# Kernel optimization log

Hardware: AMD Instinct MI355X
Metric: run time of the kernel (lower is better)

## Reference

```python
import jax, jax.numpy as jnp
import numpy as np

N = 4_194_304  # number of Gaussian samples (rays * samples_per_ray)


def setup_inputs() -> dict:
    key = jax.random.key(0)
    k1, k2 = jax.random.split(key)
    # means spread around the unit sphere so mask (||x||>=1) is mixed
    mean = jax.random.normal(k1, (N, 3), dtype=jnp.float32)
    cov = jax.random.normal(k2, (N, 3, 3), dtype=jnp.float32)
    return {"mean": mean, "cov": cov}


def _contract(x):
    # f(x) = x if ||x||<=1 else (2 - 1/||x||) * x/||x||  (Frobenius norm, order=None)
    mag = jnp.linalg.norm(x, axis=-1, keepdims=True)
    return jnp.where(mag < 1, x, (2.0 - 1.0 / mag) * (x / mag))


def _contract_gauss(x):
    # branch-free contraction used for the Jacobian (matches torch contract_gauss)
    mag = jnp.linalg.norm(x, axis=-1, keepdims=True)
    return (2.0 - 1.0 / mag) * (x / mag)


def reference(mean, cov):
    means = _contract(mean)  # [N, 3]
    # per-sample 3x3 Jacobian of contract_gauss, mirroring torch.func.vmap(jacrev(...))
    jc = jax.vmap(jax.jacrev(_contract_gauss))(mean)  # [N, 3, 3]
    mag = jnp.linalg.norm(mean, axis=-1)  # [N]
    mask = mag >= 1.0
    # J @ cov @ J^T for masked samples; computed densely then selected (same math)
    new_cov = jnp.einsum("nij,njk,nlk->nil", jc, cov, jc)
    cov_out = jnp.where(mask[:, None, None], new_cov, cov)
    return means, cov_out
```

## Files before the change

kernel.cpp:

```cpp
#include <hip/hip_runtime.h>


#define BLOCK 256

__global__ __launch_bounds__(BLOCK) void scene_contraction_kernel(
    const float* __restrict__ mean,
    const float* __restrict__ cov,
    float* __restrict__ out_mean,
    float* __restrict__ out_cov,
    int N)
{
    __shared__ float sm[BLOCK * 3];
    __shared__ float sc[BLOCK * 9];

    const int tid = threadIdx.x;
    const long long bs = (long long)blockIdx.x * BLOCK;
    const bool full = (bs + BLOCK <= (long long)N);

    if (full) {
        const float4* gm4 = (const float4*)(mean + bs * 3);
        float4* sm4 = (float4*)sm;
        if (tid < 192) sm4[tid] = gm4[tid];

        const float4* gc4 = (const float4*)(cov + bs * 9);
        float4* sc4 = (float4*)sc;
        sc4[tid]        = gc4[tid];
        sc4[tid + 256]  = gc4[tid + 256];
        if (tid < 64) sc4[tid + 512] = gc4[tid + 512];
    } else {
        const long long m_end = (long long)N * 3 - bs * 3;
        for (int i = tid; i < BLOCK * 3; i += BLOCK)
            if (i < m_end) sm[i] = mean[bs * 3 + i];
        const long long c_end = (long long)N * 9 - bs * 9;
        for (int i = tid; i < BLOCK * 9; i += BLOCK)
            if (i < c_end) sc[i] = cov[bs * 9 + i];
    }
    __syncthreads();

    if (bs + tid < (long long)N) {
        const float x = sm[tid * 3 + 0];
        const float y = sm[tid * 3 + 1];
        const float z = sm[tid * 3 + 2];
        const float r2 = x * x + y * y + z * z;
        const float r = sqrtf(r2);

        if (r >= 1.0f) {
            const float inv  = 1.0f / r;
            const float s    = (2.0f - inv) * inv;
            const float inv2 = inv * inv;
            const float cc   = 2.0f * (1.0f - r) * (inv2 * inv2);

            const float j00 = fmaf(cc * x, x, s);
            const float j01 = cc * x * y;
            const float j02 = cc * x * z;
            const float j11 = fmaf(cc * y, y, s);
            const float j12 = cc * y * z;
            const float j22 = fmaf(cc * z, z, s);

            const float e0 = sc[tid * 9 + 0], e1 = sc[tid * 9 + 1], e2 = sc[tid * 9 + 2];
            const float e3 = sc[tid * 9 + 3], e4 = sc[tid * 9 + 4], e5 = sc[tid * 9 + 5];
            const float e6 = sc[tid * 9 + 6], e7 = sc[tid * 9 + 7], e8 = sc[tid * 9 + 8];

            const float t00 = j00 * e0 + j01 * e3 + j02 * e6;
            const float t01 = j00 * e1 + j01 * e4 + j02 * e7;
            const float t02 = j00 * e2 + j01 * e5 + j02 * e8;
            const float t10 = j01 * e0 + j11 * e3 + j12 * e6;
            const float t11 = j01 * e1 + j11 * e4 + j12 * e7;
            const float t12 = j01 * e2 + j11 * e5 + j12 * e8;
            const float t20 = j02 * e0 + j12 * e3 + j22 * e6;
            const float t21 = j02 * e1 + j12 * e4 + j22 * e7;
            const float t22 = j02 * e2 + j12 * e5 + j22 * e8;

            sc[tid * 9 + 0] = t00 * j00 + t01 * j01 + t02 * j02;
            sc[tid * 9 + 1] = t00 * j01 + t01 * j11 + t02 * j12;
            sc[tid * 9 + 2] = t00 * j02 + t01 * j12 + t02 * j22;
            sc[tid * 9 + 3] = t10 * j00 + t11 * j01 + t12 * j02;
            sc[tid * 9 + 4] = t10 * j01 + t11 * j11 + t12 * j12;
            sc[tid * 9 + 5] = t10 * j02 + t11 * j12 + t12 * j22;
            sc[tid * 9 + 6] = t20 * j00 + t21 * j01 + t22 * j02;
            sc[tid * 9 + 7] = t20 * j01 + t21 * j11 + t22 * j12;
            sc[tid * 9 + 8] = t20 * j02 + t21 * j12 + t22 * j22;

            sm[tid * 3 + 0] = s * x;
            sm[tid * 3 + 1] = s * y;
            sm[tid * 3 + 2] = s * z;
        }
    }
    __syncthreads();

    if (full) {
        float4* om4 = (float4*)(out_mean + bs * 3);
        const float4* sm4 = (const float4*)sm;
        if (tid < 192) om4[tid] = sm4[tid];

        float4* oc4 = (float4*)(out_cov + bs * 9);
        const float4* sc4 = (const float4*)sc;
        oc4[tid]        = sc4[tid];
        oc4[tid + 256]  = sc4[tid + 256];
        if (tid < 64) oc4[tid + 512] = sc4[tid + 512];
    } else {
        const long long m_end = (long long)N * 3 - bs * 3;
        for (int i = tid; i < BLOCK * 3; i += BLOCK)
            if (i < m_end) out_mean[bs * 3 + i] = sm[i];
        const long long c_end = (long long)N * 9 - bs * 9;
        for (int i = tid; i < BLOCK * 9; i += BLOCK)
            if (i < c_end) out_cov[bs * 9 + i] = sc[i];
    }
}

extern "C" void kernel_launch(void* const* d_in, const int* in_sizes, int n_in,
                              void* d_out, int out_size, void* d_ws, size_t ws_size,
                              hipStream_t stream) {
    const float* mean = (const float*)d_in[0];
    const float* cov  = (const float*)d_in[1];
    float* out        = (float*)d_out;

    const int N = in_sizes[0] / 3;
    float* out_mean = out;
    float* out_cov  = out + (size_t)N * 3;

    const int blocks = (N + BLOCK - 1) / BLOCK;
    hipLaunchKernelGGL(scene_contraction_kernel, dim3(blocks), dim3(BLOCK), 0, stream,
                       mean, cov, out_mean, out_cov, N);
}
```

Baseline: 331.8 us.

## Process four samples per thread with direct float4 loads, drop LDS staging

Replaces the shared-memory staging with per-thread register processing of four consecutive samples. Each thread loads 3 float4 of means and 9 float4 of covariance directly, and the contraction becomes branch-free via select. This removes the LDS round trip and barriers and increases loads in flight per thread. The cost is strided per-lane access within a wavefront, which may hurt coalescing, and higher register use.

```diff
diff --git a/kernel.cpp b/kernel.cpp
--- a/kernel.cpp
+++ b/kernel.cpp
@@ -2,6 +2,58 @@
 
 
 #define BLOCK 256
+
+union F12 { float4 v[3]; float f[12]; };
+union F36 { float4 v[9]; float f[36]; };
+
+__device__ __forceinline__ void contract_one(
+    float x, float y, float z,
+    const float* __restrict__ e,
+    float* __restrict__ om,
+    float* __restrict__ oc)
+{
+    const float r2 = fmaf(x, x, fmaf(y, y, z * z));
+    const float r  = sqrtf(r2);
+    const float inv = 1.0f / r;
+    float s  = (2.0f - inv) * inv;
+    const float inv2 = inv * inv;
+    float cc = 2.0f * (1.0f - r) * (inv2 * inv2);
+
+    const bool inside = r < 1.0f;
+    s  = inside ? 1.0f : s;
+    cc = inside ? 0.0f : cc;
+
+    const float j00 = fmaf(cc * x, x, s);
+    const float j01 = cc * x * y;
+    const float j02 = cc * x * z;
+    const float j11 = fmaf(cc * y, y, s);
+    const float j12 = cc * y * z;
+    const float j22 = fmaf(cc * z, z, s);
+
+    om[0] = s * x;
+    om[1] = s * y;
+    om[2] = s * z;
+
+    const float t00 = j00 * e[0] + j01 * e[3] + j02 * e[6];
+    const float t01 = j00 * e[1] + j01 * e[4] + j02 * e[7];
+    const float t02 = j00 * e[2] + j01 * e[5] + j02 * e[8];
+    const float t10 = j01 * e[0] + j11 * e[3] + j12 * e[6];
+    const float t11 = j01 * e[1] + j11 * e[4] + j12 * e[7];
+    const float t12 = j01 * e[2] + j11 * e[5] + j12 * e[8];
+    const float t20 = j02 * e[0] + j12 * e[3] + j22 * e[6];
+    const float t21 = j02 * e[1] + j12 * e[4] + j22 * e[7];
+    const float t22 = j02 * e[2] + j12 * e[5] + j22 * e[8];
+
+    oc[0] = t00 * j00 + t01 * j01 + t02 * j02;
+    oc[1] = t00 * j01 + t01 * j11 + t02 * j12;
+    oc[2] = t00 * j02 + t01 * j12 + t02 * j22;
+    oc[3] = t10 * j00 + t11 * j01 + t12 * j02;
+    oc[4] = t10 * j01 + t11 * j11 + t12 * j12;
+    oc[5] = t10 * j02 + t11 * j12 + t12 * j22;
+    oc[6] = t20 * j00 + t21 * j01 + t22 * j02;
+    oc[7] = t20 * j01 + t21 * j11 + t22 * j12;
+    oc[8] = t20 * j02 + t21 * j12 + t22 * j22;
+}
 
 __global__ __launch_bounds__(BLOCK) void scene_contraction_kernel(
     const float* __restrict__ mean,
@@ -10,101 +62,43 @@
     float* __restrict__ out_cov,
     int N)
 {
-    __shared__ float sm[BLOCK * 3];
-    __shared__ float sc[BLOCK * 9];
+    const long long t  = (long long)blockIdx.x * BLOCK + threadIdx.x;
+    const long long s0 = t * 4;
+    if (s0 >= N) return;
 
-    const int tid = threadIdx.x;
-    const long long bs = (long long)blockIdx.x * BLOCK;
-    const bool full = (bs + BLOCK <= (long long)N);
+    if (s0 + 4 <= N) {
+        F12 m;  F36 c;
+        const float4* mg = (const float4*)mean + t * 3;
+        const float4* cg = (const float4*)cov  + t * 9;
+        #pragma unroll
+        for (int i = 0; i < 3; ++i) m.v[i] = mg[i];
+        #pragma unroll
+        for (int i = 0; i < 9; ++i) c.v[i] = cg[i];
 
-    if (full) {
-        const float4* gm4 = (const float4*)(mean + bs * 3);
-        float4* sm4 = (float4*)sm;
-        if (tid < 192) sm4[tid] = gm4[tid];
+        F12 om; F36 oc;
+        #pragma unroll
+        for (int k = 0; k < 4; ++k)
+            contract_one(m.f[3*k], m.f[3*k+1], m.f[3*k+2],
+                         &c.f[9*k], &om.f[3*k], &oc.f[9*k]);
 
-        const float4* gc4 = (const float4*)(cov + bs * 9);
-        float4* sc4 = (float4*)sc;
-        sc4[tid]        = gc4[tid];
-        sc4[tid + 256]  = gc4[tid + 256];
-        if (tid < 64) sc4[tid + 512] = gc4[tid + 512];
+        float4* omg = (float4*)out_mean + t * 3;
+        float4* ocg = (float4*)out_cov  + t * 9;
+        #pragma unroll
+        for (int i = 0; i < 3; ++i) omg[i] = om.v[i];
+        #pragma unroll
+        for (int i = 0; i < 9; ++i) ocg[i] = oc.v[i];
     } else {
-        const long long m_end = (long long)N * 3 - bs * 3;
-        for (int i = tid; i < BLOCK * 3; i += BLOCK)
-            if (i < m_end) sm[i] = mean[bs * 3 + i];
-        const long long c_end = (long long)N * 9 - bs * 9;
-        for (int i = tid; i < BLOCK * 9; i += BLOCK)
-            if (i < c_end) sc[i] = cov[bs * 9 + i];
-    }
-    __syncthreads();
-
-    if (bs + tid < (long long)N) {
-        const float x = sm[tid * 3 + 0];
-        const float y = sm[tid * 3 + 1];
-        const float z = sm[tid * 3 + 2];
-        const float r2 = x * x + y * y + z * z;
-        const float r = sqrtf(r2);
-
-        if (r >= 1.0f) {
-            const float inv  = 1.0f / r;
-            const float s    = (2.0f - inv) * inv;
-            const float inv2 = inv * inv;
-            const float cc   = 2.0f * (1.0f - r) * (inv2 * inv2);
-
-            const float j00 = fmaf(cc * x, x, s);
-            const float j01 = cc * x * y;
-            const float j02 = cc * x * z;
-            const float j11 = fmaf(cc * y, y, s);
-            const float j12 = cc * y * z;
-            const float j22 = fmaf(cc * z, z, s);
-
-            const float e0 = sc[tid * 9 + 0], e1 = sc[tid * 9 + 1], e2 = sc[tid * 9 + 2];
-            const float e3 = sc[tid * 9 + 3], e4 = sc[tid * 9 + 4], e5 = sc[tid * 9 + 5];
-            const float e6 = sc[tid * 9 + 6], e7 = sc[tid * 9 + 7], e8 = sc[tid * 9 + 8];
-
-            const float t00 = j00 * e0 + j01 * e3 + j02 * e6;
-            const float t01 = j00 * e1 + j01 * e4 + j02 * e7;
-            const float t02 = j00 * e2 + j01 * e5 + j02 * e8;
-            const float t10 = j01 * e0 + j11 * e3 + j12 * e6;
-            const float t11 = j01 * e1 + j11 * e4 + j12 * e7;
-            const float t12 = j01 * e2 + j11 * e5 + j12 * e8;
-            const float t20 = j02 * e0 + j12 * e3 + j22 * e6;
-            const float t21 = j02 * e1 + j12 * e4 + j22 * e7;
-            const float t22 = j02 * e2 + j12 * e5 + j22 * e8;
-
-            sc[tid * 9 + 0] = t00 * j00 + t01 * j01 + t02 * j02;
-            sc[tid * 9 + 1] = t00 * j01 + t01 * j11 + t02 * j12;
-            sc[tid * 9 + 2] = t00 * j02 + t01 * j12 + t02 * j22;
-            sc[tid * 9 + 3] = t10 * j00 + t11 * j01 + t12 * j02;
-            sc[tid * 9 + 4] = t10 * j01 + t11 * j11 + t12 * j12;
-            sc[tid * 9 + 5] = t10 * j02 + t11 * j12 + t12 * j22;
-            sc[tid * 9 + 6] = t20 * j00 + t21 * j01 + t22 * j02;
-            sc[tid * 9 + 7] = t20 * j01 + t21 * j11 + t22 * j12;
-            sc[tid * 9 + 8] = t20 * j02 + t21 * j12 + t22 * j22;
-
-            sm[tid * 3 + 0] = s * x;
-            sm[tid * 3 + 1] = s * y;
-            sm[tid * 3 + 2] = s * z;
+        for (long long sidx = s0; sidx < N; ++sidx) {
+            float e[9], om[3], oc[9];
+            #pragma unroll
+            for (int i = 0; i < 9; ++i) e[i] = cov[sidx * 9 + i];
+            contract_one(mean[sidx * 3], mean[sidx * 3 + 1], mean[sidx * 3 + 2],
+                         e, om, oc);
+            #pragma unroll
+            for (int i = 0; i < 3; ++i) out_mean[sidx * 3 + i] = om[i];
+            #pragma unroll
+            for (int i = 0; i < 9; ++i) out_cov[sidx * 9 + i] = oc[i];
         }
-    }
-    __syncthreads();
-
-    if (full) {
-        float4* om4 = (float4*)(out_mean + bs * 3);
-        const float4* sm4 = (const float4*)sm;
-        if (tid < 192) om4[tid] = sm4[tid];
-
-        float4* oc4 = (float4*)(out_cov + bs * 9);
-        const float4* sc4 = (const float4*)sc;
-        oc4[tid]        = sc4[tid];
-        oc4[tid + 256]  = sc4[tid + 256];
-        if (tid < 64) oc4[tid + 512] = sc4[tid + 512];
-    } else {
-        const long long m_end = (long long)N * 3 - bs * 3;
-        for (int i = tid; i < BLOCK * 3; i += BLOCK)
-            if (i < m_end) out_mean[bs * 3 + i] = sm[i];
-        const long long c_end = (long long)N * 9 - bs * 9;
-        for (int i = tid; i < BLOCK * 9; i += BLOCK)
-            if (i < c_end) out_cov[bs * 9 + i] = sc[i];
     }
 }
 
@@ -119,7 +113,8 @@
     float* out_mean = out;
     float* out_cov  = out + (size_t)N * 3;
 
-    const int blocks = (N + BLOCK - 1) / BLOCK;
+    const long long nthreads = ((long long)N + 3) / 4;
+    const int blocks = (int)((nthreads + BLOCK - 1) / BLOCK);
     hipLaunchKernelGGL(scene_contraction_kernel, dim3(blocks), dim3(BLOCK), 0, stream,
                        mean, cov, out_mean, out_cov, N);
 }
```

New measurement: 413.5 us. 1.25x slower.
